# Performance work log

Hardware: AMD Instinct MI355X
Metric: run time of the kernel (lower is better)

The kernel has to match this reference:

```python
import jax, jax.numpy as jnp
import numpy as np

EMBED = 1152
HEADS = 16
HEAD_DIM = EMBED // HEADS
SCALE = HEAD_DIM ** -0.5


def setup_inputs() -> dict:
    key = jax.random.key(0)
    k1, k2, k3, k4, k5 = jax.random.split(key, 5)
    B, S = 32, 729
    std = EMBED ** -0.5
    return {
        "hidden_state": jax.random.normal(k1, (B, S, EMBED), dtype=jnp.float32),
        "qkv_w": jax.random.normal(k2, (3 * EMBED, EMBED), dtype=jnp.float32) * std,
        "qkv_b": jax.random.normal(k3, (3 * EMBED,), dtype=jnp.float32) * 0.02,
        "out_w": jax.random.normal(k4, (EMBED, EMBED), dtype=jnp.float32) * std,
        "out_b": jax.random.normal(k5, (EMBED,), dtype=jnp.float32) * 0.02,
    }


def reference(hidden_state, qkv_w, qkv_b, out_w, out_b):
    B, S, _ = hidden_state.shape
    qkv = hidden_state @ qkv_w.T + qkv_b  # [B,S,3E]
    q, k, v = jnp.split(qkv, 3, axis=-1)
    # [B,S,E] -> [B,H,S,Dh]
    def heads(x):
        return x.reshape(B, S, HEADS, HEAD_DIM).transpose(0, 2, 1, 3)
    q, k, v = heads(q), heads(k), heads(v)
    scores = jnp.einsum("bhqd,bhkd->bhqk", q, k) * SCALE
    scores = jax.nn.softmax(scores, axis=-1)  # [B,H,S,S]
    out = jnp.einsum("bhqk,bhkd->bhqd", scores, v)
    out = out.transpose(0, 2, 1, 3).reshape(B, S, EMBED)
    out = out @ out_w.T + out_b
    return out, scores
```

## Files before the change

### kernel.cpp

```cpp
#include <hip/hip_runtime.h>

#define B_    32
#define S_    729
#define E_    1152
#define H_    16
#define D_    72
#define M1_   23328
#define MPAD_ 23424
#define SQ_   736
#define SK_   768
#define DP_   96
#define VR_   96
#define SCALE_ 0.11785113019775793f

typedef __attribute__((ext_vector_type(8))) _Float16 f16x8;
typedef __attribute__((ext_vector_type(4))) _Float16 f16x4;
typedef __attribute__((ext_vector_type(4))) float    f32x4;

#define GLDS16(g, l) __builtin_amdgcn_global_load_lds(                      \
    (__attribute__((address_space(1))) void*)(g),                           \
    (__attribute__((address_space(3))) void*)(l), 16, 0, 0)

union H2U { _Float16 h[2]; uint32_t u; };

__global__ void cvt_f16(const float4* __restrict__ src, f16x4* __restrict__ dst, int n4) {
  int stride = gridDim.x * blockDim.x;
  for (int i = blockIdx.x * blockDim.x + threadIdx.x; i < n4; i += stride) {
    float4 v = src[i];
    f16x4 o;
    o.x = (_Float16)v.x; o.y = (_Float16)v.y;
    o.z = (_Float16)v.z; o.w = (_Float16)v.w;
    dst[i] = o;
  }
}

template<int MODE>
__global__ __launch_bounds__(256)
void gemm_f16(const _Float16* __restrict__ A, const _Float16* __restrict__ W,
              const float* __restrict__ bias,
              _Float16* __restrict__ Qp, _Float16* __restrict__ Kp,
              _Float16* __restrict__ Vtp, float* __restrict__ Cout)
{
  __shared__ _Float16 As[128 * 64];
  __shared__ _Float16 Bs[128 * 64];
  const int tid = threadIdx.x;
  const int l  = tid & 63;
  const int wv = tid >> 6;
  const int lq = l & 15, lk = l >> 4;
  const int m0 = blockIdx.x * 128;
  const int n0 = blockIdx.y * 128;
  const int wm = (wv & 1) * 64, wn = (wv >> 1) * 64;
  const int srow = l >> 3;
  const int scol = (l & 7) * 8;

  f32x4 acc[4][4] = {};

  for (int k0 = 0; k0 < 1152; k0 += 64) {
    #pragma unroll
    for (int q = 0; q < 4; ++q) {
      int chunk = wv * 4 + q;
      int row = chunk * 8 + srow;
      GLDS16(A + (size_t)(m0 + row) * 1152 + k0 + scol, &As[chunk * 512 + l * 8]);
      GLDS16(W + (size_t)(n0 + row) * 1152 + k0 + scol, &Bs[chunk * 512 + l * 8]);
    }
    __syncthreads();
    #pragma unroll
    for (int kk = 0; kk < 64; kk += 32) {
      f16x8 a[4], b[4];
      #pragma unroll
      for (int i = 0; i < 4; ++i)
        a[i] = *(const f16x8*)&As[(wm + 16 * i + lq) * 64 + kk + lk * 8];
      #pragma unroll
      for (int j = 0; j < 4; ++j)
        b[j] = *(const f16x8*)&Bs[(wn + 16 * j + lq) * 64 + kk + lk * 8];
      #pragma unroll
      for (int i = 0; i < 4; ++i)
        #pragma unroll
        for (int j = 0; j < 4; ++j)
          acc[i][j] = __builtin_amdgcn_mfma_f32_16x16x32_f16(a[i], b[j], acc[i][j], 0, 0, 0);
    }
    __syncthreads();
  }

  #pragma unroll
  for (int i = 0; i < 4; ++i) {
    #pragma unroll
    for (int j = 0; j < 4; ++j) {
      int n = n0 + wn + 16 * j + lq;
      float bn = bias[n];
      #pragma unroll
      for (int r = 0; r < 4; ++r) {
        int m = m0 + wm + 16 * i + lk * 4 + r;
        if (m >= M1_) continue;
        float v = acc[i][j][r] + bn;
        if (MODE == 0) {
          unsigned um = (unsigned)m;
          unsigned bq = um / 729u, s = um - bq * 729u;
          unsigned un = (unsigned)n;
          unsigned which = un / 1152u, e = un - which * 1152u;
          unsigned h = e / 72u, d = e - h * 72u;
          unsigned bh = bq * 16u + h;
          if (which == 0) {
            Qp[((size_t)bh * SQ_ + s) * DP_ + d] = (_Float16)(v * SCALE_);
          } else if (which == 1) {
            Kp[((size_t)bh * SK_ + s) * DP_ + d] = (_Float16)v;
          } else {
            Vtp[((size_t)bh * VR_ + d) * 768 + s] = (_Float16)v;
          }
        } else {
          Cout[(size_t)m * 1152 + n] = v;
        }
      }
    }
  }
}

struct AttnSmem {
  union {
    char  stage[2][24576];
    float ored[4][32][96];
  };
  uint32_t pexch[8][64][4];
  float redmax[32][4];
  float redsum[32][4];
  float invl[32];
};

__global__ __launch_bounds__(512, 3)
void attn_k(const _Float16* __restrict__ Q, const _Float16* __restrict__ K,
            const _Float16* __restrict__ Vt, float* __restrict__ scores,
            _Float16* __restrict__ AO)
{
  __shared__ AttnSmem sm;
  const int tid = threadIdx.x;
  const int l   = tid & 63;
  const int wv  = tid >> 6;
  const int lq  = l & 15, lk = l >> 4;
  const int i   = wv >> 2;
  const int sl  = wv & 3;
  const int bh  = blockIdx.x;
  const int q0  = blockIdx.y * 32;
  const int b   = bh >> 4, h = bh & 15;

  const _Float16* Qb = Q  + (size_t)bh * SQ_ * DP_;
  const _Float16* Kb = K  + (size_t)bh * SK_ * DP_;
  const _Float16* Vb = Vt + (size_t)bh * VR_ * 768;

  auto stageK = [&](char* buf, int t) {
    #pragma unroll
    for (int it = 0; it < 3; ++it) {
      int s = it * 512 + tid;
      int row = s / 12, cp = s - row * 12;
      int cc = (cp < 8) ? (cp ^ (row & 7)) : (8 + ((cp & 3) ^ ((row >> 1) & 3)));
      GLDS16(Kb + (size_t)(t * 128 + row) * DP_ + cc * 8, buf + s * 16);
    }
  };
  auto stageV = [&](char* buf, int t) {
    #pragma unroll
    for (int it = 0; it < 3; ++it) {
      int s = it * 512 + tid;
      int row = s >> 4, cp = s & 15;
      int cc = cp ^ (row & 15);
      GLDS16(Vb + (size_t)row * 768 + t * 128 + cc * 8, buf + s * 16);
    }
  };

  stageK(sm.stage[0], 0);
  f16x8 aq[3];
  {
    const _Float16* qp = Qb + (size_t)(q0 + 16 * i + lq) * DP_ + lk * 8;
    aq[0] = *(const f16x8*)(qp);
    aq[1] = *(const f16x8*)(qp + 32);
    aq[2] = *(const f16x8*)(qp + 64);
  }
  asm volatile("s_waitcnt vmcnt(0)" ::: "memory");
  __builtin_amdgcn_s_barrier();

  f32x4 sacc[12] = {};
  #pragma unroll
  for (int t = 0; t < 6; ++t) {
    if (t < 5) stageK(sm.stage[(t + 1) & 1], t + 1);
    const char* bufp = sm.stage[t & 1];
    #pragma unroll
    for (int lcb = 0; lcb < 2; ++lcb) {
      int row = (2 * sl + lcb) * 16 + lq;
      #pragma unroll
      for (int t3 = 0; t3 < 3; ++t3) {
        int cc = 4 * t3 + lk;
        int cp = (cc < 8) ? (cc ^ (row & 7)) : (8 + ((cc & 3) ^ ((row >> 1) & 3)));
        f16x8 ka = *(const f16x8*)(bufp + row * 192 + cp * 16);
        sacc[2 * t + lcb] = __builtin_amdgcn_mfma_f32_16x16x32_f16(ka, aq[t3], sacc[2 * t + lcb], 0, 0, 0);
      }
    }
    asm volatile("s_waitcnt vmcnt(0)" ::: "memory");
    __builtin_amdgcn_s_barrier();
  }

  stageV(sm.stage[0], 0);

  #pragma unroll
  for (int c = 10; c < 12; ++c) {
    int kbase = (40 + 2 * sl + (c & 1)) * 16 + 4 * lk;
    #pragma unroll
    for (int r = 0; r < 4; ++r)
      if (kbase + r > 728) sacc[c][r] = -1e30f;
  }

  float m = -1e30f;
  #pragma unroll
  for (int c = 0; c < 12; ++c)
    #pragma unroll
    for (int r = 0; r < 4; ++r) m = fmaxf(m, sacc[c][r]);
  m = fmaxf(m, __shfl_xor(m, 16));
  m = fmaxf(m, __shfl_xor(m, 32));
  if (lk == 0) sm.redmax[16 * i + lq][sl] = m;
  asm volatile("s_waitcnt lgkmcnt(0)" ::: "memory");
  __builtin_amdgcn_s_barrier();
  float gm;
  { const float* rp = sm.redmax[16 * i + lq];
    gm = fmaxf(fmaxf(rp[0], rp[1]), fmaxf(rp[2], rp[3])); }

  float sum = 0.f;
  #pragma unroll
  for (int c = 0; c < 12; ++c)
    #pragma unroll
    for (int r = 0; r < 4; ++r) {
      float e = __expf(sacc[c][r] - gm);
      sacc[c][r] = e;
      sum += e;
    }
  sum += __shfl_xor(sum, 16);
  sum += __shfl_xor(sum, 32);
  if (lk == 0) sm.redsum[16 * i + lq][sl] = sum;
  asm volatile("s_waitcnt lgkmcnt(0)" ::: "memory");
  __builtin_amdgcn_s_barrier();
  float inv;
  { const float* rp = sm.redsum[16 * i + lq];
    inv = 1.0f / (rp[0] + rp[1] + rp[2] + rp[3]); }
  if (lk == 0 && sl == 0) sm.invl[16 * i + lq] = inv;

  {
    const int q = q0 + 16 * i + lq;
    if (q < S_) {
      float* sc = scores + (size_t)bh * S_ * S_ + (size_t)q * S_;
      #pragma unroll
      for (int c = 0; c < 12; ++c) {
        int k0 = (8 * (c >> 1) + 2 * sl + (c & 1)) * 16 + 4 * lk;
        f32x4 v = sacc[c] * inv;
        if (k0 + 3 <= 728)      *(f32x4*)(sc + k0) = v;
        else if (k0 == 728)     sc[728] = v[0];
      }
    }
  }

  uint32_t pk[12][2];
  #pragma unroll
  for (int c = 0; c < 12; ++c) {
    H2U a0, a1;
    a0.h[0] = (_Float16)sacc[c][0]; a0.h[1] = (_Float16)sacc[c][1];
    a1.h[0] = (_Float16)sacc[c][2]; a1.h[1] = (_Float16)sacc[c][3];
    pk[c][0] = a0.u; pk[c][1] = a1.u;
  }

  asm volatile("s_waitcnt vmcnt(0)" ::: "memory");
  __builtin_amdgcn_s_barrier();

  f32x4 oacc[6] = {};
  const int srcA = lq + 16 * (2 * (lk & 1));
  const int srcB = srcA + 16;
  #pragma unroll
  for (int t = 0; t < 6; ++t) {
    if (t < 5) stageV(sm.stage[(t + 1) & 1], t + 1);
    uint4 w = make_uint4(pk[2 * t][0], pk[2 * t][1], pk[2 * t + 1][0], pk[2 * t + 1][1]);
    *(uint4*)&sm.pexch[wv][l][0] = w;
    asm volatile("s_waitcnt lgkmcnt(0)" ::: "memory");
    __builtin_amdgcn_sched_barrier(0);
    uint2 dA = *(const uint2*)((const char*)&sm.pexch[wv][srcA][0] + (lk >> 1) * 8);
    uint2 dB = *(const uint2*)((const char*)&sm.pexch[wv][srcB][0] + (lk >> 1) * 8);
    uint4 pad4 = make_uint4(dA.x, dA.y, dB.x, dB.y);
    f16x8 pa = __builtin_bit_cast(f16x8, pad4);

    const char* bufp = sm.stage[t & 1];
    #pragma unroll
    for (int db = 0; db < 6; ++db) {
      int row = db * 16 + lq;
      int cc = 4 * sl + lk;
      int cp = cc ^ (row & 15);
      f16x8 bv = *(const f16x8*)(bufp + row * 256 + cp * 16);
      oacc[db] = __builtin_amdgcn_mfma_f32_16x16x32_f16(pa, bv, oacc[db], 0, 0, 0);
    }
    asm volatile("s_waitcnt vmcnt(0)" ::: "memory");
    __builtin_amdgcn_s_barrier();
  }

  #pragma unroll
  for (int db = 0; db < 6; ++db)
    #pragma unroll
    for (int r = 0; r < 4; ++r)
      sm.ored[sl][16 * i + lk * 4 + r][db * 16 + lq] = oacc[db][r];
  asm volatile("s_waitcnt lgkmcnt(0)" ::: "memory");
  __builtin_amdgcn_s_barrier();

  {
    int qq = tid >> 4, dc = tid & 15;
    int qglob = q0 + qq;
    if (dc < 12 && qglob < S_) {
      int d0 = dc * 6;
      float iv = sm.invl[qq];
      _Float16* ap = AO + ((size_t)(b * S_ + qglob)) * E_ + h * D_ + d0;
      #pragma unroll
      for (int e = 0; e < 6; ++e) {
        float v = sm.ored[0][qq][d0 + e] + sm.ored[1][qq][d0 + e]
                + sm.ored[2][qq][d0 + e] + sm.ored[3][qq][d0 + e];
        ap[e] = (_Float16)(v * iv);
      }
    }
  }
}

extern "C" void kernel_launch(void* const* d_in, const int* in_sizes, int n_in,
                              void* d_out, int out_size, void* d_ws, size_t ws_size,
                              hipStream_t stream)
{
  const float* hidden = (const float*)d_in[0];
  const float* qkv_w  = (const float*)d_in[1];
  const float* qkv_b  = (const float*)d_in[2];
  const float* out_w  = (const float*)d_in[3];
  const float* out_b  = (const float*)d_in[4];
  float* out    = (float*)d_out;
  float* scores = out + (size_t)M1_ * E_;

  char* ws = (char*)d_ws;
  const size_t szA1 = (size_t)MPAD_ * 1152 * 2;
  const size_t szWq = (size_t)3456 * 1152 * 2;
  const size_t szWo = (size_t)1152 * 1152 * 2;
  const size_t szQ  = (size_t)512 * SQ_ * DP_ * 2;
  const size_t szK  = (size_t)512 * SK_ * DP_ * 2;
  const size_t szV  = (size_t)512 * VR_ * 768 * 2;
  const size_t offA1 = 0;
  const size_t offWq = offA1 + szA1;
  const size_t offWo = offWq + szWq;
  const size_t offQ  = offWo + szWo;
  const size_t offK  = offQ  + szQ;
  const size_t offVt = offK  + szK;
  const size_t need  = offVt + szV;
  if (ws_size < need) return;

  _Float16* A1  = (_Float16*)(ws + offA1);
  _Float16* Wq  = (_Float16*)(ws + offWq);
  _Float16* Wo  = (_Float16*)(ws + offWo);
  _Float16* Qp  = (_Float16*)(ws + offQ);
  _Float16* Kp  = (_Float16*)(ws + offK);
  _Float16* Vtp = (_Float16*)(ws + offVt);
  _Float16* AO  = A1;

  hipMemsetAsync(Qp,  0, szQ, stream);
  hipMemsetAsync(Kp,  0, szK, stream);
  hipMemsetAsync(Vtp, 0, szV, stream);

  cvt_f16<<<26244, 256, 0, stream>>>((const float4*)hidden, (f16x4*)A1, (M1_ * E_) / 4);
  cvt_f16<<<3888,  256, 0, stream>>>((const float4*)qkv_w,  (f16x4*)Wq, (3456 * 1152) / 4);
  cvt_f16<<<1296,  256, 0, stream>>>((const float4*)out_w,  (f16x4*)Wo, (1152 * 1152) / 4);

  gemm_f16<0><<<dim3(183, 27), 256, 0, stream>>>(A1, Wq, qkv_b, Qp, Kp, Vtp, nullptr);
  attn_k<<<dim3(512, 23), 512, 0, stream>>>(Qp, Kp, Vtp, scores, AO);
  gemm_f16<1><<<dim3(183, 9), 256, 0, stream>>>(AO, Wo, out_b, nullptr, nullptr, nullptr, out);
}
```

Baseline: 1.274 ms.

## Load K and V directly from global in attention, dropping LDS staging

The attention kernel no longer stages K and V tiles through double-buffered shared memory with per-tile barriers. Each wave now reads its K and V fragments straight from global memory. The grid is transposed so that the 23 query tiles of the same batch-head are adjacent, which should keep K and V hot in cache. Freeing the staging buffers lets the launch bound ask for 4 blocks per SM, and the memsets of Q and Vt are removed. The trade-off is less coalesced global reads, and padded Vt columns are no longer zeroed, so leftover garbage there could propagate.

```diff
diff --git a/kernel.cpp b/kernel.cpp
--- a/kernel.cpp
+++ b/kernel.cpp
@@ -116,17 +116,14 @@
 }
 
 struct AttnSmem {
-  union {
-    char  stage[2][24576];
-    float ored[4][32][96];
-  };
+  float ored[4][32][96];
   uint32_t pexch[8][64][4];
   float redmax[32][4];
   float redsum[32][4];
   float invl[32];
 };
 
-__global__ __launch_bounds__(512, 3)
+__global__ __launch_bounds__(512, 4)
 void attn_k(const _Float16* __restrict__ Q, const _Float16* __restrict__ K,
             const _Float16* __restrict__ Vt, float* __restrict__ scores,
             _Float16* __restrict__ AO)
@@ -138,34 +135,15 @@
   const int lq  = l & 15, lk = l >> 4;
   const int i   = wv >> 2;
   const int sl  = wv & 3;
-  const int bh  = blockIdx.x;
-  const int q0  = blockIdx.y * 32;
+  const int qt  = blockIdx.x;
+  const int bh  = blockIdx.y;
+  const int q0  = qt * 32;
   const int b   = bh >> 4, h = bh & 15;
 
   const _Float16* Qb = Q  + (size_t)bh * SQ_ * DP_;
   const _Float16* Kb = K  + (size_t)bh * SK_ * DP_;
   const _Float16* Vb = Vt + (size_t)bh * VR_ * 768;
 
-  auto stageK = [&](char* buf, int t) {
-    #pragma unroll
-    for (int it = 0; it < 3; ++it) {
-      int s = it * 512 + tid;
-      int row = s / 12, cp = s - row * 12;
-      int cc = (cp < 8) ? (cp ^ (row & 7)) : (8 + ((cp & 3) ^ ((row >> 1) & 3)));
-      GLDS16(Kb + (size_t)(t * 128 + row) * DP_ + cc * 8, buf + s * 16);
-    }
-  };
-  auto stageV = [&](char* buf, int t) {
-    #pragma unroll
-    for (int it = 0; it < 3; ++it) {
-      int s = it * 512 + tid;
-      int row = s >> 4, cp = s & 15;
-      int cc = cp ^ (row & 15);
-      GLDS16(Vb + (size_t)row * 768 + t * 128 + cc * 8, buf + s * 16);
-    }
-  };
-
-  stageK(sm.stage[0], 0);
   f16x8 aq[3];
   {
     const _Float16* qp = Qb + (size_t)(q0 + 16 * i + lq) * DP_ + lk * 8;
@@ -173,30 +151,19 @@
     aq[1] = *(const f16x8*)(qp + 32);
     aq[2] = *(const f16x8*)(qp + 64);
   }
-  asm volatile("s_waitcnt vmcnt(0)" ::: "memory");
-  __builtin_amdgcn_s_barrier();
 
   f32x4 sacc[12] = {};
   #pragma unroll
-  for (int t = 0; t < 6; ++t) {
-    if (t < 5) stageK(sm.stage[(t + 1) & 1], t + 1);
-    const char* bufp = sm.stage[t & 1];
-    #pragma unroll
-    for (int lcb = 0; lcb < 2; ++lcb) {
-      int row = (2 * sl + lcb) * 16 + lq;
-      #pragma unroll
-      for (int t3 = 0; t3 < 3; ++t3) {
-        int cc = 4 * t3 + lk;
-        int cp = (cc < 8) ? (cc ^ (row & 7)) : (8 + ((cc & 3) ^ ((row >> 1) & 3)));
-        f16x8 ka = *(const f16x8*)(bufp + row * 192 + cp * 16);
-        sacc[2 * t + lcb] = __builtin_amdgcn_mfma_f32_16x16x32_f16(ka, aq[t3], sacc[2 * t + lcb], 0, 0, 0);
-      }
-    }
-    asm volatile("s_waitcnt vmcnt(0)" ::: "memory");
-    __builtin_amdgcn_s_barrier();
-  }
-
-  stageV(sm.stage[0], 0);
+  for (int c = 0; c < 12; ++c) {
+    int cb = 8 * (c >> 1) + 2 * sl + (c & 1);
+    const _Float16* kp = Kb + (size_t)(cb * 16 + lq) * DP_ + lk * 8;
+    f16x8 k0 = *(const f16x8*)(kp);
+    f16x8 k1 = *(const f16x8*)(kp + 32);
+    f16x8 k2 = *(const f16x8*)(kp + 64);
+    sacc[c] = __builtin_amdgcn_mfma_f32_16x16x32_f16(k0, aq[0], sacc[c], 0, 0, 0);
+    sacc[c] = __builtin_amdgcn_mfma_f32_16x16x32_f16(k1, aq[1], sacc[c], 0, 0, 0);
+    sacc[c] = __builtin_amdgcn_mfma_f32_16x16x32_f16(k2, aq[2], sacc[c], 0, 0, 0);
+  }
 
   #pragma unroll
   for (int c = 10; c < 12; ++c) {
@@ -262,15 +229,11 @@
     pk[c][0] = a0.u; pk[c][1] = a1.u;
   }
 
-  asm volatile("s_waitcnt vmcnt(0)" ::: "memory");
-  __builtin_amdgcn_s_barrier();
-
   f32x4 oacc[6] = {};
   const int srcA = lq + 16 * (2 * (lk & 1));
   const int srcB = srcA + 16;
   #pragma unroll
   for (int t = 0; t < 6; ++t) {
-    if (t < 5) stageV(sm.stage[(t + 1) & 1], t + 1);
     uint4 w = make_uint4(pk[2 * t][0], pk[2 * t][1], pk[2 * t + 1][0], pk[2 * t + 1][1]);
     *(uint4*)&sm.pexch[wv][l][0] = w;
     asm volatile("s_waitcnt lgkmcnt(0)" ::: "memory");
@@ -280,17 +243,12 @@
     uint4 pad4 = make_uint4(dA.x, dA.y, dB.x, dB.y);
     f16x8 pa = __builtin_bit_cast(f16x8, pad4);
 
-    const char* bufp = sm.stage[t & 1];
     #pragma unroll
     for (int db = 0; db < 6; ++db) {
-      int row = db * 16 + lq;
-      int cc = 4 * sl + lk;
-      int cp = cc ^ (row & 15);
-      f16x8 bv = *(const f16x8*)(bufp + row * 256 + cp * 16);
+      const _Float16* vp = Vb + (size_t)(db * 16 + lq) * 768 + t * 128 + (4 * sl + lk) * 8;
+      f16x8 bv = *(const f16x8*)(vp);
       oacc[db] = __builtin_amdgcn_mfma_f32_16x16x32_f16(pa, bv, oacc[db], 0, 0, 0);
     }
-    asm volatile("s_waitcnt vmcnt(0)" ::: "memory");
-    __builtin_amdgcn_s_barrier();
   }
 
   #pragma unroll
@@ -354,15 +312,13 @@
   _Float16* Vtp = (_Float16*)(ws + offVt);
   _Float16* AO  = A1;
 
-  hipMemsetAsync(Qp,  0, szQ, stream);
-  hipMemsetAsync(Kp,  0, szK, stream);
-  hipMemsetAsync(Vtp, 0, szV, stream);
+  hipMemsetAsync(Kp, 0, szK, stream);
 
   cvt_f16<<<26244, 256, 0, stream>>>((const float4*)hidden, (f16x4*)A1, (M1_ * E_) / 4);
   cvt_f16<<<3888,  256, 0, stream>>>((const float4*)qkv_w,  (f16x4*)Wq, (3456 * 1152) / 4);
   cvt_f16<<<1296,  256, 0, stream>>>((const float4*)out_w,  (f16x4*)Wo, (1152 * 1152) / 4);
 
   gemm_f16<0><<<dim3(183, 27), 256, 0, stream>>>(A1, Wq, qkv_b, Qp, Kp, Vtp, nullptr);
-  attn_k<<<dim3(512, 23), 512, 0, stream>>>(Qp, Kp, Vtp, scores, AO);
+  attn_k<<<dim3(23, 512), 512, 0, stream>>>(Qp, Kp, Vtp, scores, AO);
   gemm_f16<1><<<dim3(183, 9), 256, 0, stream>>>(AO, Wo, out_b, nullptr, nullptr, nullptr, out);
 }
```

Result: slower. 1.535 ms (+20.5%).

## Pipeline K/V staging two tiles ahead and remap blocks per XCD in attention

Applied to the files above, without the earlier changes.

Restructures the attention kernel's staging into one unified K-then-V tile stream that prefetches two tiles ahead, waiting with partial vmcnt so global loads overlap the MFMA work. Block indices become a 1D grid remapped so that blocks for the same (batch, head) land on the same XCD, aiming for better L2 reuse of K/V. Scores are now written after the PV loop from the fp16-packed probabilities, the occupancy hint rises to 4, and the output reduction buffer gets an XOR swizzle to cut LDS bank conflicts. The risks are that scores lose precision by going through fp16, and that the tighter register budget may cause spills.

```diff
diff --git a/kernel.cpp b/kernel.cpp
--- a/kernel.cpp
+++ b/kernel.cpp
@@ -126,7 +126,7 @@
   float invl[32];
 };
 
-__global__ __launch_bounds__(512, 3)
+__global__ __launch_bounds__(512, 4)
 void attn_k(const _Float16* __restrict__ Q, const _Float16* __restrict__ K,
             const _Float16* __restrict__ Vt, float* __restrict__ scores,
             _Float16* __restrict__ AO)
@@ -138,34 +138,42 @@
   const int lq  = l & 15, lk = l >> 4;
   const int i   = wv >> 2;
   const int sl  = wv & 3;
-  const int bh  = blockIdx.x;
-  const int q0  = blockIdx.y * 32;
-  const int b   = bh >> 4, h = bh & 15;
+  const int p    = blockIdx.x;
+  const int xcd  = p & 7;
+  const int slot = p >> 3;
+  const int hl   = slot / 23;
+  const int qt   = slot - hl * 23;
+  const int bh   = hl * 8 + xcd;
+  const int q0   = qt * 32;
+  const int b    = bh >> 4, h = bh & 15;
 
   const _Float16* Qb = Q  + (size_t)bh * SQ_ * DP_;
   const _Float16* Kb = K  + (size_t)bh * SK_ * DP_;
   const _Float16* Vb = Vt + (size_t)bh * VR_ * 768;
 
-  auto stageK = [&](char* buf, int t) {
-    #pragma unroll
-    for (int it = 0; it < 3; ++it) {
-      int s = it * 512 + tid;
-      int row = s / 12, cp = s - row * 12;
-      int cc = (cp < 8) ? (cp ^ (row & 7)) : (8 + ((cp & 3) ^ ((row >> 1) & 3)));
-      GLDS16(Kb + (size_t)(t * 128 + row) * DP_ + cc * 8, buf + s * 16);
+  auto stage = [&](int idx) {
+    char* buf = sm.stage[idx & 1];
+    if (idx < 6) {
+      #pragma unroll
+      for (int it = 0; it < 3; ++it) {
+        int s = it * 512 + tid;
+        int row = s / 12, cp = s - row * 12;
+        int cc = (cp < 8) ? (cp ^ (row & 7)) : (8 + ((cp & 3) ^ ((row >> 1) & 3)));
+        GLDS16(Kb + (size_t)(idx * 128 + row) * DP_ + cc * 8, buf + s * 16);
+      }
+    } else {
+      #pragma unroll
+      for (int it = 0; it < 3; ++it) {
+        int s = it * 512 + tid;
+        int row = s >> 4, cp = s & 15;
+        int cc = cp ^ (row & 15);
+        GLDS16(Vb + (size_t)row * 768 + (idx - 6) * 128 + cc * 8, buf + s * 16);
+      }
     }
   };
-  auto stageV = [&](char* buf, int t) {
-    #pragma unroll
-    for (int it = 0; it < 3; ++it) {
-      int s = it * 512 + tid;
-      int row = s >> 4, cp = s & 15;
-      int cc = cp ^ (row & 15);
-      GLDS16(Vb + (size_t)row * 768 + t * 128 + cc * 8, buf + s * 16);
-    }
-  };
-
-  stageK(sm.stage[0], 0);
+
+  stage(0);
+  stage(1);
   f16x8 aq[3];
   {
     const _Float16* qp = Qb + (size_t)(q0 + 16 * i + lq) * DP_ + lk * 8;
@@ -179,7 +187,8 @@
   f32x4 sacc[12] = {};
   #pragma unroll
   for (int t = 0; t < 6; ++t) {
-    if (t < 5) stageK(sm.stage[(t + 1) & 1], t + 1);
+    asm volatile("s_waitcnt vmcnt(3)" ::: "memory");
+    __builtin_amdgcn_s_barrier();
     const char* bufp = sm.stage[t & 1];
     #pragma unroll
     for (int lcb = 0; lcb < 2; ++lcb) {
@@ -192,11 +201,10 @@
         sacc[2 * t + lcb] = __builtin_amdgcn_mfma_f32_16x16x32_f16(ka, aq[t3], sacc[2 * t + lcb], 0, 0, 0);
       }
     }
-    asm volatile("s_waitcnt vmcnt(0)" ::: "memory");
+    asm volatile("s_waitcnt lgkmcnt(0)" ::: "memory");
     __builtin_amdgcn_s_barrier();
-  }
-
-  stageV(sm.stage[0], 0);
+    stage(t + 2);
+  }
 
   #pragma unroll
   for (int c = 10; c < 12; ++c) {
@@ -239,20 +247,6 @@
     inv = 1.0f / (rp[0] + rp[1] + rp[2] + rp[3]); }
   if (lk == 0 && sl == 0) sm.invl[16 * i + lq] = inv;
 
-  {
-    const int q = q0 + 16 * i + lq;
-    if (q < S_) {
-      float* sc = scores + (size_t)bh * S_ * S_ + (size_t)q * S_;
-      #pragma unroll
-      for (int c = 0; c < 12; ++c) {
-        int k0 = (8 * (c >> 1) + 2 * sl + (c & 1)) * 16 + 4 * lk;
-        f32x4 v = sacc[c] * inv;
-        if (k0 + 3 <= 728)      *(f32x4*)(sc + k0) = v;
-        else if (k0 == 728)     sc[728] = v[0];
-      }
-    }
-  }
-
   uint32_t pk[12][2];
   #pragma unroll
   for (int c = 0; c < 12; ++c) {
@@ -262,16 +256,15 @@
     pk[c][0] = a0.u; pk[c][1] = a1.u;
   }
 
-  asm volatile("s_waitcnt vmcnt(0)" ::: "memory");
-  __builtin_amdgcn_s_barrier();
-
   f32x4 oacc[6] = {};
   const int srcA = lq + 16 * (2 * (lk & 1));
   const int srcB = srcA + 16;
   #pragma unroll
-  for (int t = 0; t < 6; ++t) {
-    if (t < 5) stageV(sm.stage[(t + 1) & 1], t + 1);
-    uint4 w = make_uint4(pk[2 * t][0], pk[2 * t][1], pk[2 * t + 1][0], pk[2 * t + 1][1]);
+  for (int v = 0; v < 6; ++v) {
+    if (v < 5) { asm volatile("s_waitcnt vmcnt(3)" ::: "memory"); }
+    else       { asm volatile("s_waitcnt vmcnt(0)" ::: "memory"); }
+    __builtin_amdgcn_s_barrier();
+    uint4 w = make_uint4(pk[2 * v][0], pk[2 * v][1], pk[2 * v + 1][0], pk[2 * v + 1][1]);
     *(uint4*)&sm.pexch[wv][l][0] = w;
     asm volatile("s_waitcnt lgkmcnt(0)" ::: "memory");
     __builtin_amdgcn_sched_barrier(0);
@@ -280,7 +273,7 @@
     uint4 pad4 = make_uint4(dA.x, dA.y, dB.x, dB.y);
     f16x8 pa = __builtin_bit_cast(f16x8, pad4);
 
-    const char* bufp = sm.stage[t & 1];
+    const char* bufp = sm.stage[v & 1];
     #pragma unroll
     for (int db = 0; db < 6; ++db) {
       int row = db * 16 + lq;
@@ -289,15 +282,36 @@
       f16x8 bv = *(const f16x8*)(bufp + row * 256 + cp * 16);
       oacc[db] = __builtin_amdgcn_mfma_f32_16x16x32_f16(pa, bv, oacc[db], 0, 0, 0);
     }
-    asm volatile("s_waitcnt vmcnt(0)" ::: "memory");
+    asm volatile("s_waitcnt lgkmcnt(0)" ::: "memory");
     __builtin_amdgcn_s_barrier();
+    if (v < 4) stage(v + 8);
   }
 
   #pragma unroll
   for (int db = 0; db < 6; ++db)
     #pragma unroll
-    for (int r = 0; r < 4; ++r)
-      sm.ored[sl][16 * i + lk * 4 + r][db * 16 + lq] = oacc[db][r];
+    for (int r = 0; r < 4; ++r) {
+      int row = 16 * i + lk * 4 + r;
+      sm.ored[sl][row][(db * 16 + lq) ^ (row & 12)] = oacc[db][r];
+    }
+
+  {
+    const int q = q0 + 16 * i + lq;
+    if (q < S_) {
+      float* sc = scores + (size_t)bh * S_ * S_ + (size_t)q * S_;
+      #pragma unroll
+      for (int c = 0; c < 12; ++c) {
+        int k0 = (8 * (c >> 1) + 2 * sl + (c & 1)) * 16 + 4 * lk;
+        H2U u0, u1; u0.u = pk[c][0]; u1.u = pk[c][1];
+        f32x4 vv;
+        vv[0] = (float)u0.h[0] * inv; vv[1] = (float)u0.h[1] * inv;
+        vv[2] = (float)u1.h[0] * inv; vv[3] = (float)u1.h[1] * inv;
+        if (k0 + 3 <= 728)  *(f32x4*)(sc + k0) = vv;
+        else if (k0 == 728) sc[728] = vv[0];
+      }
+    }
+  }
+
   asm volatile("s_waitcnt lgkmcnt(0)" ::: "memory");
   __builtin_amdgcn_s_barrier();
 
@@ -310,8 +324,9 @@
       _Float16* ap = AO + ((size_t)(b * S_ + qglob)) * E_ + h * D_ + d0;
       #pragma unroll
       for (int e = 0; e < 6; ++e) {
-        float v = sm.ored[0][qq][d0 + e] + sm.ored[1][qq][d0 + e]
-                + sm.ored[2][qq][d0 + e] + sm.ored[3][qq][d0 + e];
+        int col = (d0 + e) ^ (qq & 12);
+        float v = sm.ored[0][qq][col] + sm.ored[1][qq][col]
+                + sm.ored[2][qq][col] + sm.ored[3][qq][col];
         ap[e] = (_Float16)(v * iv);
       }
     }
@@ -363,6 +378,6 @@
   cvt_f16<<<1296,  256, 0, stream>>>((const float4*)out_w,  (f16x4*)Wo, (1152 * 1152) / 4);
 
   gemm_f16<0><<<dim3(183, 27), 256, 0, stream>>>(A1, Wq, qkv_b, Qp, Kp, Vtp, nullptr);
-  attn_k<<<dim3(512, 23), 512, 0, stream>>>(Qp, Kp, Vtp, scores, AO);
+  attn_k<<<11776, 512, 0, stream>>>(Qp, Kp, Vtp, scores, AO);
   gemm_f16<1><<<dim3(183, 9), 256, 0, stream>>>(AO, Wo, out_b, nullptr, nullptr, nullptr, out);
 }
```

Measured after the change: 1.174 ms. -7.8%, faster.
